# Kernel tuning notes

Measured on AMD Instinct MI355X. Metric: run time of the kernel, lower is better.

## Reference

```python
import jax, jax.numpy as jnp
import numpy as np

N = 100000   # nodes
E = 1600000  # directed edges (before self loops)
IN = 64
HID = 32     # per-head hidden channels
H = 4        # heads
OUT = 32     # final output channels
NEG_SLOPE = 0.2
LN_EPS = 1e-5


def setup_inputs() -> dict:
    key = jax.random.key(0)
    ks = jax.random.split(key, 24)
    def nrm(k, shape, s=0.1):
        return jax.random.normal(k, shape, jnp.float32) * s
    inp = {
        "x": jax.random.normal(ks[0], (N, IN), jnp.float32),
        "edge_index": jax.random.randint(ks[1], (2, E), 0, N, jnp.int32),
    }
    in_dims = [IN, H * HID, H * HID]
    j = 2
    for i, di in enumerate(in_dims):
        inp[f"W{i}"] = nrm(ks[j], (di, H * HID)); j += 1
        inp[f"as{i}"] = nrm(ks[j], (H, HID)); j += 1
        inp[f"ad{i}"] = nrm(ks[j], (H, HID)); j += 1
        inp[f"b{i}"] = jnp.zeros((H * HID,), jnp.float32)
        inp[f"g{i}"] = jnp.ones((H * HID,), jnp.float32)
        inp[f"be{i}"] = jnp.zeros((H * HID,), jnp.float32)
    inp["Wf"] = nrm(ks[j], (H * HID, OUT)); j += 1
    inp["asf"] = nrm(ks[j], (1, OUT)); j += 1
    inp["adf"] = nrm(ks[j], (1, OUT)); j += 1
    inp["bf"] = jnp.zeros((OUT,), jnp.float32)
    return inp


def gat_conv(x, src, dst, W, att_s, att_d, bias, heads, C, concat, n_nodes):
    # h: [N, H, C]
    h = (x @ W).reshape(n_nodes, heads, C)
    a_src = jnp.sum(h * att_s, axis=-1)  # [N, H]
    a_dst = jnp.sum(h * att_d, axis=-1)  # [N, H]
    e = jax.nn.leaky_relu(a_src[src] + a_dst[dst], NEG_SLOPE)  # [E', H]
    # segment softmax over incoming edges of each dst node
    m = jax.ops.segment_max(e, dst, num_segments=n_nodes)
    m = jnp.where(jnp.isfinite(m), m, 0.0)
    ex = jnp.exp(e - m[dst])
    denom = jax.ops.segment_sum(ex, dst, num_segments=n_nodes)
    alpha = ex / (denom[dst] + 1e-16)  # [E', H]
    msg = h[src] * alpha[..., None]    # [E', H, C]
    out = jax.ops.segment_sum(msg, dst, num_segments=n_nodes)  # [N, H, C]
    if concat:
        out = out.reshape(n_nodes, heads * C)
    else:
        out = out.mean(axis=1)
    return out + bias


def layer_norm(x, g, b):
    mu = x.mean(-1, keepdims=True)
    v = jnp.mean((x - mu) ** 2, axis=-1, keepdims=True)
    return g * (x - mu) / jnp.sqrt(v + LN_EPS) + b


def reference(x, edge_index,
              W0, as0, ad0, b0, g0, be0,
              W1, as1, ad1, b1, g1, be1,
              W2, as2, ad2, b2, g2, be2,
              Wf, asf, adf, bf):
    n_nodes = x.shape[0]
    loop = jnp.arange(n_nodes, dtype=edge_index.dtype)
    src = jnp.concatenate([edge_index[0], loop])  # add self loops (PyG default)
    dst = jnp.concatenate([edge_index[1], loop])
    blocks = [(W0, as0, ad0, b0, g0, be0),
              (W1, as1, ad1, b1, g1, be1),
              (W2, as2, ad2, b2, g2, be2)]
    for (W, a_s, a_d, b, g, be) in blocks:
        x = gat_conv(x, src, dst, W, a_s, a_d, b, H, HID, True, n_nodes)
        x = jax.nn.elu(layer_norm(x, g, be))
    return gat_conv(x, src, dst, Wf, asf, adf, bf, 1, OUT, False, n_nodes)
```

## Files before the change

kernel.cpp:

```cpp
#include <hip/hip_runtime.h>
#include <hip/hip_bf16.h>

constexpr int NN   = 100000;
constexpr int EE   = 1600000;
constexpr int ETOT = EE + NN;
constexpr float SLOPE = 0.2f;
constexpr int BSH = 8;
constexpr int NB  = (NN + (1 << BSH) - 1) >> BSH;
constexpr int CCH = 8192;
constexpr int DCAP  = 36;
constexpr int DCAPP = 37;

typedef __attribute__((ext_vector_type(8))) short short8;
typedef __attribute__((ext_vector_type(4))) float f32x4;

__device__ __forceinline__ float bf_lo(unsigned u) { return __uint_as_float(u << 16); }
__device__ __forceinline__ float bf_hi(unsigned u) { return __uint_as_float(u & 0xffff0000u); }
__device__ __forceinline__ unsigned short f2bf(float f) {
    __hip_bfloat16 h = __float2bfloat16(f);
    return *(unsigned short*)&h;
}
__device__ __forceinline__ void wave_lds_fence() {
    __asm__ volatile("s_waitcnt lgkmcnt(0)" ::: "memory");
}
__device__ __forceinline__ void fma8(float* acc, uint4 u, float al) {
    acc[0] += bf_lo(u.x) * al; acc[1] += bf_hi(u.x) * al;
    acc[2] += bf_lo(u.y) * al; acc[3] += bf_hi(u.y) * al;
    acc[4] += bf_lo(u.z) * al; acc[5] += bf_hi(u.z) * al;
    acc[6] += bf_lo(u.w) * al; acc[7] += bf_hi(u.w) * al;
}
__device__ __forceinline__ void fma4(float* acc, uint2 u, float al) {
    acc[0] += bf_lo(u.x) * al; acc[1] += bf_hi(u.x) * al;
    acc[2] += bf_lo(u.y) * al; acc[3] += bf_hi(u.y) * al;
}

__global__ void k_cvt_x(const float* __restrict__ x, unsigned short* __restrict__ xb) {
    int i = blockIdx.x * blockDim.x + threadIdx.x;
    if (i >= NN * 64 / 8) return;
    const float4* xp = (const float4*)(x + (size_t)i * 8);
    float4 v0 = xp[0], v1 = xp[1];
    unsigned short o[8] = {f2bf(v0.x), f2bf(v0.y), f2bf(v0.z), f2bf(v0.w),
                           f2bf(v1.x), f2bf(v1.y), f2bf(v1.z), f2bf(v1.w)};
    *(uint4*)(xb + (size_t)i * 8) = *(uint4*)o;
}

__global__ void k_cvt_wt(const float* __restrict__ W, unsigned short* __restrict__ Wt,
                         int K, int N) {
    int i = blockIdx.x * blockDim.x + threadIdx.x;
    if (i >= K * N) return;
    int k = i / N, n = i % N;
    Wt[(size_t)n * K + k] = f2bf(W[i]);
}

__global__ void k_zero(int* p, int n) {
    int i = blockIdx.x * blockDim.x + threadIdx.x;
    if (i < n) p[i] = 0;
}

__global__ __launch_bounds__(256) void k_bhist(const int* __restrict__ ei,
                                               int* __restrict__ gbh) {
    __shared__ int h[NB];
    int t = threadIdx.x;
    for (int i = t; i < NB; i += 256) h[i] = 0;
    __syncthreads();
    int i = blockIdx.x * 2048 + t;
#pragma unroll
    for (int k = 0; k < 8; k++, i += 256)
        if (i < EE) atomicAdd(&h[ei[EE + i] >> BSH], 1);
    __syncthreads();
    for (int j = t; j < NB; j += 256)
        if (h[j]) atomicAdd(&gbh[j], h[j]);
}

__global__ void k_bscan(const int* __restrict__ gbh, int* __restrict__ ebase,
                        int* __restrict__ gcur) {
    __shared__ int sd[512];
    int t = threadIdx.x;
    int v = (t < NB) ? gbh[t] : 0;
    sd[t] = v;
    __syncthreads();
    for (int off = 1; off < 512; off <<= 1) {
        int x = (t >= off) ? sd[t - off] : 0;
        __syncthreads();
        sd[t] += x;
        __syncthreads();
    }
    int ex = sd[t] - v;
    if (t < NB) { ebase[t] = ex; gcur[t] = ex; }
    if (t == NB) ebase[NB] = EE;
}

__global__ __launch_bounds__(256) void k_bscatter(const int* __restrict__ ei,
                                                  int* __restrict__ gcur,
                                                  int* __restrict__ pbuf) {
    __shared__ int h[NB], base[NB], cur[NB];
    int t = threadIdx.x;
    for (int i = t; i < NB; i += 256) { h[i] = 0; cur[i] = 0; }
    __syncthreads();
    int c0 = blockIdx.x * CCH;
    int cend = c0 + CCH < EE ? c0 + CCH : EE;
    for (int i = c0 + t; i < cend; i += 256)
        atomicAdd(&h[ei[EE + i] >> BSH], 1);
    __syncthreads();
    for (int i = t; i < NB; i += 256)
        if (h[i] > 0) base[i] = atomicAdd(&gcur[i], h[i]);
    __syncthreads();
    for (int i = c0 + t; i < cend; i += 256) {
        int s = ei[i], d = ei[EE + i];
        int b = d >> BSH;
        int c = atomicAdd(&cur[b], 1);
        pbuf[base[b] + c] = s | ((d & ((1 << BSH) - 1)) << 17);
    }
}

__global__ __launch_bounds__(256) void k_bcsr(const int* __restrict__ pbuf,
                                              const int* __restrict__ ebase,
                                              int* __restrict__ row_ptr,
                                              int* __restrict__ esrc) {
    constexpr int BNODES = 1 << BSH;
    __shared__ int hist[BNODES];
    __shared__ int cur[BNODES];
    __shared__ int sd[256];
    int b = blockIdx.x, t = threadIdx.x;
    int node0 = b << BSH;
    int e0 = ebase[b], e1 = ebase[b + 1];
    hist[t] = 0; cur[t] = 0;
    __syncthreads();
    for (int i = e0 + t; i < e1; i += 256)
        atomicAdd(&hist[pbuf[i] >> 17], 1);
    __syncthreads();
    int ts = hist[t];
    sd[t] = ts;
    __syncthreads();
    for (int off = 1; off < 256; off <<= 1) {
        int x = (t >= off) ? sd[t - off] : 0;
        __syncthreads();
        sd[t] += x;
        __syncthreads();
    }
    int ex = sd[t] - ts;
    __syncthreads();
    hist[t] = ex;
    __syncthreads();
    int rbase = e0 + node0;
    int n = node0 + t;
    if (n < NN) {
        int rp = rbase + hist[t] + t;
        row_ptr[n] = rp;
        esrc[rp] = n;
    }
    __syncthreads();
    for (int i = e0 + t; i < e1; i += 256) {
        int p = pbuf[i];
        int nl = p >> 17;
        int c = atomicAdd(&cur[nl], 1);
        esrc[rbase + hist[nl] + nl + 1 + c] = p & 0x1FFFF;
    }
}

template <int BN, int H>
__global__ __launch_bounds__(256) void k_mfma_att(
    const unsigned short* __restrict__ Ab, const unsigned short* __restrict__ Bt,
    const float* __restrict__ as_, const float* __restrict__ ad_,
    unsigned short* __restrict__ hb, float* __restrict__ a_s,
    float* __restrict__ a_d, int M, int K) {
    constexpr int NCT = BN / 16;
    constexpr int LDK = 72;
    __shared__ unsigned short As[128 * LDK];
    __shared__ unsigned short Bs[BN * LDK];
    int tid = threadIdx.x;
    int lane = tid & 63, w = tid >> 6;
    int q = lane >> 4, col = lane & 15;
    int rowBase = blockIdx.x * 128;

    f32x4 acc[2][NCT];
#pragma unroll
    for (int rt = 0; rt < 2; rt++)
#pragma unroll
        for (int ct = 0; ct < NCT; ct++) acc[rt][ct] = (f32x4){0.f, 0.f, 0.f, 0.f};

    int u = tid & 7;
    int r0 = tid >> 3;
    int nph = K >> 6;
    for (int ph = 0; ph < nph; ph++) {
        int kof = ph * 64 + u * 8;
#pragma unroll
        for (int rr = r0; rr < 128; rr += 32) {
            int gr = rowBase + rr;
            uint4 v = make_uint4(0, 0, 0, 0);
            if (gr < M) v = *(const uint4*)(Ab + (size_t)gr * K + kof);
            *(uint4*)(&As[rr * LDK + u * 8]) = v;
        }
#pragma unroll
        for (int br = r0; br < BN; br += 32) {
            uint4 v = *(const uint4*)(Bt + (size_t)br * K + kof);
            *(uint4*)(&Bs[br * LDK + u * 8]) = v;
        }
        __syncthreads();

        short8 af[2][2];
#pragma unroll
        for (int rt = 0; rt < 2; rt++)
#pragma unroll
            for (int kt = 0; kt < 2; kt++)
                af[rt][kt] = *(const short8*)(&As[(w * 32 + rt * 16 + col) * LDK + kt * 32 + q * 8]);
#pragma unroll
        for (int kt = 0; kt < 2; kt++)
#pragma unroll
            for (int ct = 0; ct < NCT; ct++) {
                short8 bf = *(const short8*)(&Bs[(ct * 16 + col) * LDK + kt * 32 + q * 8]);
#pragma unroll
                for (int rt = 0; rt < 2; rt++)
                    acc[rt][ct] = __builtin_amdgcn_mfma_f32_16x16x32_bf16(
                        af[rt][kt], bf, acc[rt][ct], 0, 0, 0);
            }
        __syncthreads();
    }

    float swv[NCT], dwv[NCT];
#pragma unroll
    for (int ct = 0; ct < NCT; ct++) {
        int c = ct * 16 + col;
        swv[ct] = as_[c];
        dwv[ct] = ad_[c];
    }
#pragma unroll
    for (int rt = 0; rt < 2; rt++) {
#pragma unroll
        for (int r = 0; r < 4; r++) {
            int gr = rowBase + w * 32 + rt * 16 + q * 4 + r;
            if constexpr (H == 4) {
                float ps[4] = {0, 0, 0, 0}, pd[4] = {0, 0, 0, 0};
#pragma unroll
                for (int ct = 0; ct < NCT; ct++) {
                    float v = acc[rt][ct][r];
                    ps[ct >> 1] += v * swv[ct];
                    pd[ct >> 1] += v * dwv[ct];
                }
#pragma unroll
                for (int m = 1; m < 16; m <<= 1)
#pragma unroll
                    for (int h = 0; h < 4; h++) {
                        ps[h] += __shfl_xor(ps[h], m);
                        pd[h] += __shfl_xor(pd[h], m);
                    }
                if (gr < M) {
#pragma unroll
                    for (int ct = 0; ct < NCT; ct++)
                        hb[(size_t)gr * BN + ct * 16 + col] = f2bf(acc[rt][ct][r]);
                    if (col == 0) {
                        *(float4*)(a_s + (size_t)gr * 4) = make_float4(ps[0], ps[1], ps[2], ps[3]);
                        *(float4*)(a_d + (size_t)gr * 4) = make_float4(pd[0], pd[1], pd[2], pd[3]);
                    }
                }
            } else {
                float ps = 0.f, pd = 0.f;
#pragma unroll
                for (int ct = 0; ct < NCT; ct++) {
                    float v = acc[rt][ct][r];
                    ps += v * swv[ct];
                    pd += v * dwv[ct];
                }
#pragma unroll
                for (int m = 1; m < 16; m <<= 1) {
                    ps += __shfl_xor(ps, m);
                    pd += __shfl_xor(pd, m);
                }
                if (gr < M) {
#pragma unroll
                    for (int ct = 0; ct < NCT; ct++)
                        hb[(size_t)gr * BN + ct * 16 + col] = f2bf(acc[rt][ct][r]);
                    if (col == 0) { a_s[gr] = ps; a_d[gr] = pd; }
                }
            }
        }
    }
}

__global__ __launch_bounds__(128) void k_aggregate_ln(
    const unsigned short* __restrict__ hb, const float* __restrict__ a_src,
    const float* __restrict__ a_dst, const int* __restrict__ row_ptr,
    const int* __restrict__ esrc, const float* __restrict__ bias,
    const float* __restrict__ gamma, const float* __restrict__ beta,
    unsigned short* __restrict__ xb) {
    __shared__ uint2 slab_all[2][4 * 4 * DCAPP];
    int tid = threadIdx.x;
    int w = tid >> 6, lane = tid & 63;
    int g = lane >> 4, i = lane & 15;
    int myhead = i >> 2;
    uint2* slab = slab_all[w];
    int n0 = blockIdx.x * 8 + w * 4;
    int n = n0 + g;
    bool valid = n < NN;
    int start = 0, deg = 0;
    if (valid) {
        start = row_ptr[n];
        int end = (n == NN - 1) ? ETOT : row_ptr[n + 1];
        deg = end - start;
    }
    int wmax = deg;
#pragma unroll
    for (int m = 1; m < 64; m <<= 1) wmax = max(wmax, __shfl_xor(wmax, m));

    if (wmax <= DCAP) {
        float4 ad = make_float4(0.f, 0.f, 0.f, 0.f);
        if (valid) ad = ((const float4*)a_dst)[n];
        float d0 = 0.f, d1 = 0.f, d2 = 0.f, d3 = 0.f;
        uint2* nslab = slab + g * (4 * DCAPP);
        for (int k = i; k < deg; k += 16) {
            int s = esrc[start + k];
            float4 a = ((const float4*)a_src)[s];
            float e0 = a.x + ad.x; e0 = fmaxf(e0, SLOPE * e0); float x0 = __expf(e0);
            float e1 = a.y + ad.y; e1 = fmaxf(e1, SLOPE * e1); float x1 = __expf(e1);
            float e2 = a.z + ad.z; e2 = fmaxf(e2, SLOPE * e2); float x2 = __expf(e2);
            float e3 = a.w + ad.w; e3 = fmaxf(e3, SLOPE * e3); float x3 = __expf(e3);
            nslab[0 * DCAPP + k] = make_uint2((unsigned)s, __float_as_uint(x0));
            nslab[1 * DCAPP + k] = make_uint2((unsigned)s, __float_as_uint(x1));
            nslab[2 * DCAPP + k] = make_uint2((unsigned)s, __float_as_uint(x2));
            nslab[3 * DCAPP + k] = make_uint2((unsigned)s, __float_as_uint(x3));
            d0 += x0; d1 += x1; d2 += x2; d3 += x3;
        }
#pragma unroll
        for (int m = 1; m < 16; m <<= 1) {
            d0 += __shfl_xor(d0, m);
            d1 += __shfl_xor(d1, m);
            d2 += __shfl_xor(d2, m);
            d3 += __shfl_xor(d3, m);
        }
        float dh = myhead == 0 ? d0 : myhead == 1 ? d1 : myhead == 2 ? d2 : d3;
        float inv = 1.f / (dh + 1e-16f);
        wave_lds_fence();

        float acc[8];
#pragma unroll
        for (int k = 0; k < 8; k++) acc[k] = 0.f;
        const uint2* myrow = nslab + myhead * DCAPP;
        const unsigned short* hbase = hb + i * 8;
        int j = 0;
        for (; j + 4 <= deg; j += 4) {
            uint2 p0 = myrow[j], p1 = myrow[j + 1], p2 = myrow[j + 2], p3 = myrow[j + 3];
            uint4 u0 = *(const uint4*)(hbase + (size_t)p0.x * 128);
            uint4 u1 = *(const uint4*)(hbase + (size_t)p1.x * 128);
            uint4 u2 = *(const uint4*)(hbase + (size_t)p2.x * 128);
            uint4 u3 = *(const uint4*)(hbase + (size_t)p3.x * 128);
            fma8(acc, u0, __uint_as_float(p0.y));
            fma8(acc, u1, __uint_as_float(p1.y));
            fma8(acc, u2, __uint_as_float(p2.y));
            fma8(acc, u3, __uint_as_float(p3.y));
        }
        for (; j < deg; j++) {
            uint2 p = myrow[j];
            uint4 uu = *(const uint4*)(hbase + (size_t)p.x * 128);
            fma8(acc, uu, __uint_as_float(p.y));
        }
#pragma unroll
        for (int k = 0; k < 8; k++) acc[k] *= inv;

        if (valid) {
            float y[8];
            float sum = 0.f;
            const float4* bp = (const float4*)(bias + i * 8);
            float4 b0 = bp[0], b1 = bp[1];
#pragma unroll
            for (int k = 0; k < 8; k++) {
                float b = k < 4 ? (&b0.x)[k] : (&b1.x)[k - 4];
                y[k] = acc[k] + b;
                sum += y[k];
            }
#pragma unroll
            for (int m = 1; m < 16; m <<= 1) sum += __shfl_xor(sum, m);
            float mu = sum * (1.f / 128.f);
            float ss = 0.f;
            float d[8];
#pragma unroll
            for (int k = 0; k < 8; k++) { d[k] = y[k] - mu; ss += d[k] * d[k]; }
#pragma unroll
            for (int m = 1; m < 16; m <<= 1) ss += __shfl_xor(ss, m);
            float is = rsqrtf(ss * (1.f / 128.f) + 1e-5f);
            const float4* gp = (const float4*)(gamma + i * 8);
            const float4* ep = (const float4*)(beta + i * 8);
            float4 g0 = gp[0], g1 = gp[1], e0 = ep[0], e1 = ep[1];
            unsigned short o16[8];
#pragma unroll
            for (int k = 0; k < 8; k++) {
                float gm = k < 4 ? (&g0.x)[k] : (&g1.x)[k - 4];
                float bt = k < 4 ? (&e0.x)[k] : (&e1.x)[k - 4];
                float z = gm * (d[k] * is) + bt;
                o16[k] = f2bf(z > 0.f ? z : __expf(z) - 1.f);
            }
            *(uint4*)(xb + (size_t)n * 128 + i * 8) = *(uint4*)o16;
        }
    } else {
        for (int m4 = 0; m4 < 4; m4++) {
            int nm = n0 + m4;
            if (nm >= NN) continue;
            int startm = row_ptr[nm];
            int endm = (nm == NN - 1) ? ETOT : row_ptr[nm + 1];
            int degm = endm - startm;
            float4 ad = ((const float4*)a_dst)[nm];
            int gg = lane >> 4, c16 = lane & 15, hh = c16 >> 2;
            float acc[8];
#pragma unroll
            for (int k = 0; k < 8; k++) acc[k] = 0.f;
            if (degm <= 64) {
                int msrc = 0;
                float me0 = 0.f, me1 = 0.f, me2 = 0.f, me3 = 0.f;
                if (lane < degm) {
                    int s = esrc[startm + lane];
                    msrc = s;
                    float4 a = ((const float4*)a_src)[s];
                    float e0 = a.x + ad.x; e0 = fmaxf(e0, SLOPE * e0); me0 = __expf(e0);
                    float e1 = a.y + ad.y; e1 = fmaxf(e1, SLOPE * e1); me1 = __expf(e1);
                    float e2 = a.z + ad.z; e2 = fmaxf(e2, SLOPE * e2); me2 = __expf(e2);
                    float e3 = a.w + ad.w; e3 = fmaxf(e3, SLOPE * e3); me3 = __expf(e3);
                }
                float d0 = me0, d1 = me1, d2 = me2, d3 = me3;
#pragma unroll
                for (int m = 1; m < 64; m <<= 1) {
                    d0 += __shfl_xor(d0, m);
                    d1 += __shfl_xor(d1, m);
                    d2 += __shfl_xor(d2, m);
                    d3 += __shfl_xor(d3, m);
                }
                me0 *= 1.f / (d0 + 1e-16f);
                me1 *= 1.f / (d1 + 1e-16f);
                me2 *= 1.f / (d2 + 1e-16f);
                me3 *= 1.f / (d3 + 1e-16f);
                int iters = (degm + 3) >> 2;
                for (int it = 0; it < iters; it++) {
                    int j = gg + (it << 2);
                    int jj = j < degm ? j : 0;
                    int s = __shfl(msrc, jj);
                    float a0 = __shfl(me0, jj), a1 = __shfl(me1, jj);
                    float a2 = __shfl(me2, jj), a3 = __shfl(me3, jj);
                    if (j < degm) {
                        float al = hh == 0 ? a0 : hh == 1 ? a1 : hh == 2 ? a2 : a3;
                        uint4 uu = *(const uint4*)(hb + (size_t)s * 128 + c16 * 8);
                        fma8(acc, uu, al);
                    }
                }
            } else {
                float d0 = 0.f, d1 = 0.f, d2 = 0.f, d3 = 0.f;
                for (int k = startm + lane; k < endm; k += 64) {
                    int s = esrc[k];
                    float4 a = ((const float4*)a_src)[s];
                    float e0 = a.x + ad.x; e0 = fmaxf(e0, SLOPE * e0); d0 += __expf(e0);
                    float e1 = a.y + ad.y; e1 = fmaxf(e1, SLOPE * e1); d1 += __expf(e1);
                    float e2 = a.z + ad.z; e2 = fmaxf(e2, SLOPE * e2); d2 += __expf(e2);
                    float e3 = a.w + ad.w; e3 = fmaxf(e3, SLOPE * e3); d3 += __expf(e3);
                }
#pragma unroll
                for (int m = 1; m < 64; m <<= 1) {
                    d0 += __shfl_xor(d0, m);
                    d1 += __shfl_xor(d1, m);
                    d2 += __shfl_xor(d2, m);
                    d3 += __shfl_xor(d3, m);
                }
                float invh = hh == 0 ? 1.f / (d0 + 1e-16f) : hh == 1 ? 1.f / (d1 + 1e-16f)
                           : hh == 2 ? 1.f / (d2 + 1e-16f) : 1.f / (d3 + 1e-16f);
                float adh = hh == 0 ? ad.x : hh == 1 ? ad.y : hh == 2 ? ad.z : ad.w;
                for (int j = gg; j < degm; j += 4) {
                    int s = esrc[startm + j];
                    float e = a_src[(size_t)s * 4 + hh] + adh;
                    e = fmaxf(e, SLOPE * e);
                    float al = __expf(e) * invh;
                    uint4 uu = *(const uint4*)(hb + (size_t)s * 128 + c16 * 8);
                    fma8(acc, uu, al);
                }
            }
#pragma unroll
            for (int k = 0; k < 8; k++) {
                acc[k] += __shfl_xor(acc[k], 16);
                acc[k] += __shfl_xor(acc[k], 32);
            }
            if (lane < 16) {
                float y[8];
                float sum = 0.f;
                const float4* bp = (const float4*)(bias + lane * 8);
                float4 b0 = bp[0], b1 = bp[1];
#pragma unroll
                for (int k = 0; k < 8; k++) {
                    float b = k < 4 ? (&b0.x)[k] : (&b1.x)[k - 4];
                    y[k] = acc[k] + b;
                    sum += y[k];
                }
#pragma unroll
                for (int m = 1; m < 16; m <<= 1) sum += __shfl_xor(sum, m);
                float mu = sum * (1.f / 128.f);
                float ss = 0.f;
                float d[8];
#pragma unroll
                for (int k = 0; k < 8; k++) { d[k] = y[k] - mu; ss += d[k] * d[k]; }
#pragma unroll
                for (int m = 1; m < 16; m <<= 1) ss += __shfl_xor(ss, m);
                float is = rsqrtf(ss * (1.f / 128.f) + 1e-5f);
                const float4* gp = (const float4*)(gamma + lane * 8);
                const float4* ep = (const float4*)(beta + lane * 8);
                float4 g0 = gp[0], g1 = gp[1], e0 = ep[0], e1 = ep[1];
                unsigned short o16[8];
#pragma unroll
                for (int k = 0; k < 8; k++) {
                    float gm = k < 4 ? (&g0.x)[k] : (&g1.x)[k - 4];
                    float bt = k < 4 ? (&e0.x)[k] : (&e1.x)[k - 4];
                    float z = gm * (d[k] * is) + bt;
                    o16[k] = f2bf(z > 0.f ? z : __expf(z) - 1.f);
                }
                *(uint4*)(xb + (size_t)nm * 128 + lane * 8) = *(uint4*)o16;
            }
        }
    }
}

__global__ __launch_bounds__(128) void k_agg_final(
    const unsigned short* __restrict__ hb, const float* __restrict__ a_src,
    const float* __restrict__ a_dst, const int* __restrict__ row_ptr,
    const int* __restrict__ esrc, const float* __restrict__ bf,
    float* __restrict__ out) {
    __shared__ uint2 slab_all[2][64];
    int lane = threadIdx.x & 63;
    int w = threadIdx.x >> 6;
    uint2* slab = slab_all[w];
    int n = blockIdx.x * 2 + w;
    if (n >= NN) return;
    int start = row_ptr[n];
    int end = (n == NN - 1) ? ETOT : row_ptr[n + 1];
    int deg = end - start;
    float adn = a_dst[n];

    int g = lane >> 3, c8 = lane & 7;
    float acc[4] = {0.f, 0.f, 0.f, 0.f};
    float inv = 1.f;

    if (deg <= 64) {
        int msrc = 0;
        float me = 0.f;
        if (lane < deg) {
            int s = esrc[start + lane];
            msrc = s;
            float e = a_src[s] + adn;
            e = fmaxf(e, SLOPE * e);
            me = __expf(e);
        }
        float d = me;
#pragma unroll
        for (int m = 1; m < 64; m <<= 1) d += __shfl_xor(d, m);
        inv = 1.f / (d + 1e-16f);
        if (lane < deg) slab[lane] = make_uint2((unsigned)msrc, __float_as_uint(me));
        wave_lds_fence();
        const unsigned short* hbase = hb + c8 * 4;
        int j = g;
        for (; j + 8 < deg; j += 16) {
            uint2 p0 = slab[j], p1 = slab[j + 8];
            uint2 u0 = *(const uint2*)(hbase + (size_t)p0.x * 32);
            uint2 u1 = *(const uint2*)(hbase + (size_t)p1.x * 32);
            fma4(acc, u0, __uint_as_float(p0.y));
            fma4(acc, u1, __uint_as_float(p1.y));
        }
        if (j < deg) {
            uint2 p = slab[j];
            uint2 u = *(const uint2*)(hbase + (size_t)p.x * 32);
            fma4(acc, u, __uint_as_float(p.y));
        }
#pragma unroll
        for (int k = 0; k < 4; k++) acc[k] *= inv;
    } else {
        float d = 0.f;
        for (int k = start + lane; k < end; k += 64) {
            int s = esrc[k];
            float e = a_src[s] + adn;
            e = fmaxf(e, SLOPE * e);
            d += __expf(e);
        }
#pragma unroll
        for (int m = 1; m < 64; m <<= 1) d += __shfl_xor(d, m);
        inv = 1.f / (d + 1e-16f);
        for (int j = g; j < deg; j += 8) {
            int s = esrc[start + j];
            float e = a_src[s] + adn;
            e = fmaxf(e, SLOPE * e);
            float al = __expf(e) * inv;
            uint2 u = *(const uint2*)(hb + (size_t)s * 32 + c8 * 4);
            fma4(acc, u, al);
        }
    }
#pragma unroll
    for (int k = 0; k < 4; k++) {
        acc[k] += __shfl_xor(acc[k], 8);
        acc[k] += __shfl_xor(acc[k], 16);
        acc[k] += __shfl_xor(acc[k], 32);
    }
    if (lane < 8) {
        float4 b4 = ((const float4*)bf)[lane];
        float4 o = make_float4(acc[0] + b4.x, acc[1] + b4.y, acc[2] + b4.z,
                               acc[3] + b4.w);
        ((float4*)out)[(size_t)n * 8 + lane] = o;
    }
}

extern "C" void kernel_launch(void* const* d_in, const int* in_sizes, int n_in,
                              void* d_out, int out_size, void* d_ws,
                              size_t ws_size, hipStream_t stream) {
    const float* x  = (const float*)d_in[0];
    const int* ei   = (const int*)d_in[1];
    const float* W[3]  = {(const float*)d_in[2], (const float*)d_in[8],  (const float*)d_in[14]};
    const float* AS[3] = {(const float*)d_in[3], (const float*)d_in[9],  (const float*)d_in[15]};
    const float* AD[3] = {(const float*)d_in[4], (const float*)d_in[10], (const float*)d_in[16]};
    const float* Bb[3] = {(const float*)d_in[5], (const float*)d_in[11], (const float*)d_in[17]};
    const float* G[3]  = {(const float*)d_in[6], (const float*)d_in[12], (const float*)d_in[18]};
    const float* BE[3] = {(const float*)d_in[7], (const float*)d_in[13], (const float*)d_in[19]};
    const float* Wf  = (const float*)d_in[20];
    const float* asf = (const float*)d_in[21];
    const float* adf = (const float*)d_in[22];
    const float* bfp = (const float*)d_in[23];
    float* out = (float*)d_out;

    unsigned short* xb = (unsigned short*)d_ws;
    unsigned short* hb = xb + (size_t)NN * 128;
    float* a_s = (float*)(hb + (size_t)NN * 128);
    float* a_d = a_s + (size_t)NN * 4;
    int* row_ptr = (int*)(a_d + (size_t)NN * 4);
    int* esrc    = row_ptr + NN;
    int* gbh     = esrc + ETOT;
    int* ebase   = gbh + NB;
    int* gcur    = ebase + NB + 1;
    int* pbuf    = gcur + NB;
    unsigned short* Wt0 = (unsigned short*)(pbuf + EE);
    unsigned short* Wt1 = Wt0 + 128 * 64;
    unsigned short* Wt2 = Wt1 + 128 * 128;
    unsigned short* Wtf = Wt2 + 128 * 128;

    k_cvt_x<<<(NN * 64 / 8 + 255) / 256, 256, 0, stream>>>(x, xb);
    k_cvt_wt<<<(64 * 128 + 255) / 256, 256, 0, stream>>>(W[0], Wt0, 64, 128);
    k_cvt_wt<<<(128 * 128 + 255) / 256, 256, 0, stream>>>(W[1], Wt1, 128, 128);
    k_cvt_wt<<<(128 * 128 + 255) / 256, 256, 0, stream>>>(W[2], Wt2, 128, 128);
    k_cvt_wt<<<(128 * 32 + 255) / 256, 256, 0, stream>>>(Wf, Wtf, 128, 32);

    k_zero<<<(NB + 127) / 128, 128, 0, stream>>>(gbh, NB);
    k_bhist<<<(EE + 2047) / 2048, 256, 0, stream>>>(ei, gbh);
    k_bscan<<<1, 512, 0, stream>>>(gbh, ebase, gcur);
    k_bscatter<<<(EE + CCH - 1) / CCH, 256, 0, stream>>>(ei, gcur, pbuf);
    k_bcsr<<<NB, 256, 0, stream>>>(pbuf, ebase, row_ptr, esrc);

    const unsigned short* Wts[3] = {Wt0, Wt1, Wt2};
    int K = 64;
    int gblk = (NN + 127) / 128;
    for (int l = 0; l < 3; l++) {
        k_mfma_att<128, 4><<<gblk, 256, 0, stream>>>(xb, Wts[l], AS[l], AD[l],
                                                     hb, a_s, a_d, NN, K);
        k_aggregate_ln<<<(NN + 7) / 8, 128, 0, stream>>>(hb, a_s, a_d, row_ptr,
                                                         esrc, Bb[l], G[l], BE[l], xb);
        K = 128;
    }
    k_mfma_att<32, 1><<<gblk, 256, 0, stream>>>(xb, Wtf, asf, adf, hb, a_s, a_d,
                                                NN, 128);
    k_agg_final<<<(NN + 1) / 2, 128, 0, stream>>>(hb, a_s, a_d, row_ptr, esrc,
                                                  bfp, out);
}
```

Before: 532.3 us.

## Sort nodes by degree for aggregation load balance and merge weight conversions

Builds a degree histogram during CSR construction, then scans and scatters it to get a permutation of nodes sorted by descending in-degree (clamped at 63). The aggregation kernels now process nodes in that order, so nodes handled by the same wave have similar degree and fewer lanes sit idle on the wave-max degree loop. It also merges the four weight-transpose launches into one kernel. The cost is two extra small kernels, an indirection load per node, and less locality in the output writes and row_ptr reads.

```diff
diff --git a/kernel.cpp b/kernel.cpp
--- a/kernel.cpp
+++ b/kernel.cpp
@@ -44,12 +44,25 @@
     *(uint4*)(xb + (size_t)i * 8) = *(uint4*)o;
 }
 
-__global__ void k_cvt_wt(const float* __restrict__ W, unsigned short* __restrict__ Wt,
-                         int K, int N) {
-    int i = blockIdx.x * blockDim.x + threadIdx.x;
-    if (i >= K * N) return;
-    int k = i / N, n = i % N;
-    Wt[(size_t)n * K + k] = f2bf(W[i]);
+__global__ __launch_bounds__(256) void k_cvt_w_all(
+    const float* __restrict__ W0, const float* __restrict__ W1,
+    const float* __restrict__ W2, const float* __restrict__ Wf,
+    unsigned short* __restrict__ Wt0, unsigned short* __restrict__ Wt1,
+    unsigned short* __restrict__ Wt2, unsigned short* __restrict__ Wtf) {
+    int i = blockIdx.x * 256 + threadIdx.x;
+    if (i < 8192) {
+        int k = i / 128, n = i % 128;
+        Wt0[n * 64 + k] = f2bf(W0[i]);
+    } else if (i < 24576) {
+        int j = i - 8192; int k = j / 128, n = j % 128;
+        Wt1[n * 128 + k] = f2bf(W1[j]);
+    } else if (i < 40960) {
+        int j = i - 24576; int k = j / 128, n = j % 128;
+        Wt2[n * 128 + k] = f2bf(W2[j]);
+    } else if (i < 45056) {
+        int j = i - 40960; int k = j / 32, n = j % 32;
+        Wtf[n * 128 + k] = f2bf(Wf[j]);
+    }
 }
 
 __global__ void k_zero(int* p, int n) {
@@ -73,9 +86,10 @@
 }
 
 __global__ void k_bscan(const int* __restrict__ gbh, int* __restrict__ ebase,
-                        int* __restrict__ gcur) {
+                        int* __restrict__ gcur, int* __restrict__ dh) {
     __shared__ int sd[512];
     int t = threadIdx.x;
+    if (t < 64) dh[t] = 0;
     int v = (t < NB) ? gbh[t] : 0;
     sd[t] = v;
     __syncthreads();
@@ -116,7 +130,8 @@
 __global__ __launch_bounds__(256) void k_bcsr(const int* __restrict__ pbuf,
                                               const int* __restrict__ ebase,
                                               int* __restrict__ row_ptr,
-                                              int* __restrict__ esrc) {
+                                              int* __restrict__ esrc,
+                                              int* __restrict__ dh) {
     constexpr int BNODES = 1 << BSH;
     __shared__ int hist[BNODES];
     __shared__ int cur[BNODES];
@@ -130,6 +145,10 @@
         atomicAdd(&hist[pbuf[i] >> 17], 1);
     __syncthreads();
     int ts = hist[t];
+    if (node0 + t < NN) {
+        int deg = ts + 1;
+        atomicAdd(&dh[deg > 63 ? 63 : deg], 1);
+    }
     sd[t] = ts;
     __syncthreads();
     for (int off = 1; off < 256; off <<= 1) {
@@ -155,6 +174,45 @@
         int nl = p >> 17;
         int c = atomicAdd(&cur[nl], 1);
         esrc[rbase + hist[nl] + nl + 1 + c] = p & 0x1FFFF;
+    }
+}
+
+__global__ void k_dscan(const int* __restrict__ dh, int* __restrict__ dcur) {
+    __shared__ int sd[64];
+    int t = threadIdx.x;
+    int b = 63 - t;
+    int v = dh[b];
+    sd[t] = v;
+    __syncthreads();
+    for (int off = 1; off < 64; off <<= 1) {
+        int x = (t >= off) ? sd[t - off] : 0;
+        __syncthreads();
+        sd[t] += x;
+        __syncthreads();
+    }
+    dcur[b] = sd[t] - v;
+}
+
+__global__ __launch_bounds__(256) void k_dscatter(const int* __restrict__ row_ptr,
+                                                  int* __restrict__ dcur,
+                                                  int* __restrict__ dperm) {
+    __shared__ int h[64], base[64], lcur[64];
+    int t = threadIdx.x;
+    if (t < 64) { h[t] = 0; lcur[t] = 0; }
+    __syncthreads();
+    int n = blockIdx.x * 256 + t;
+    int bin = 0;
+    if (n < NN) {
+        int deg = ((n == NN - 1) ? ETOT : row_ptr[n + 1]) - row_ptr[n];
+        bin = deg > 63 ? 63 : deg;
+        atomicAdd(&h[bin], 1);
+    }
+    __syncthreads();
+    if (t < 64 && h[t] > 0) base[t] = atomicAdd(&dcur[t], h[t]);
+    __syncthreads();
+    if (n < NN) {
+        int c = atomicAdd(&lcur[bin], 1);
+        dperm[base[bin] + c] = n;
     }
 }
 
@@ -280,7 +338,8 @@
 __global__ __launch_bounds__(128) void k_aggregate_ln(
     const unsigned short* __restrict__ hb, const float* __restrict__ a_src,
     const float* __restrict__ a_dst, const int* __restrict__ row_ptr,
-    const int* __restrict__ esrc, const float* __restrict__ bias,
+    const int* __restrict__ esrc, const int* __restrict__ dperm,
+    const float* __restrict__ bias,
     const float* __restrict__ gamma, const float* __restrict__ beta,
     unsigned short* __restrict__ xb) {
     __shared__ uint2 slab_all[2][4 * 4 * DCAPP];
@@ -290,10 +349,11 @@
     int myhead = i >> 2;
     uint2* slab = slab_all[w];
     int n0 = blockIdx.x * 8 + w * 4;
-    int n = n0 + g;
-    bool valid = n < NN;
-    int start = 0, deg = 0;
+    int idx = n0 + g;
+    bool valid = idx < NN;
+    int n = 0, start = 0, deg = 0;
     if (valid) {
+        n = dperm[idx];
         start = row_ptr[n];
         int end = (n == NN - 1) ? ETOT : row_ptr[n + 1];
         deg = end - start;
@@ -392,8 +452,9 @@
         }
     } else {
         for (int m4 = 0; m4 < 4; m4++) {
-            int nm = n0 + m4;
-            if (nm >= NN) continue;
+            int nmidx = n0 + m4;
+            if (nmidx >= NN) continue;
+            int nm = dperm[nmidx];
             int startm = row_ptr[nm];
             int endm = (nm == NN - 1) ? ETOT : row_ptr[nm + 1];
             int degm = endm - startm;
@@ -514,14 +575,15 @@
 __global__ __launch_bounds__(128) void k_agg_final(
     const unsigned short* __restrict__ hb, const float* __restrict__ a_src,
     const float* __restrict__ a_dst, const int* __restrict__ row_ptr,
-    const int* __restrict__ esrc, const float* __restrict__ bf,
-    float* __restrict__ out) {
+    const int* __restrict__ esrc, const int* __restrict__ dperm,
+    const float* __restrict__ bf, float* __restrict__ out) {
     __shared__ uint2 slab_all[2][64];
     int lane = threadIdx.x & 63;
     int w = threadIdx.x >> 6;
     uint2* slab = slab_all[w];
-    int n = blockIdx.x * 2 + w;
-    if (n >= NN) return;
+    int nidx = blockIdx.x * 2 + w;
+    if (nidx >= NN) return;
+    int n = dperm[nidx];
     int start = row_ptr[n];
     int end = (n == NN - 1) ? ETOT : row_ptr[n + 1];
     int deg = end - start;
@@ -628,18 +690,20 @@
     unsigned short* Wt1 = Wt0 + 128 * 64;
     unsigned short* Wt2 = Wt1 + 128 * 128;
     unsigned short* Wtf = Wt2 + 128 * 128;
+    int* dh    = (int*)(Wtf + 32 * 128);
+    int* dcur  = dh + 64;
+    int* dperm = dcur + 64;
 
     k_cvt_x<<<(NN * 64 / 8 + 255) / 256, 256, 0, stream>>>(x, xb);
-    k_cvt_wt<<<(64 * 128 + 255) / 256, 256, 0, stream>>>(W[0], Wt0, 64, 128);
-    k_cvt_wt<<<(128 * 128 + 255) / 256, 256, 0, stream>>>(W[1], Wt1, 128, 128);
-    k_cvt_wt<<<(128 * 128 + 255) / 256, 256, 0, stream>>>(W[2], Wt2, 128, 128);
-    k_cvt_wt<<<(128 * 32 + 255) / 256, 256, 0, stream>>>(Wf, Wtf, 128, 32);
+    k_cvt_w_all<<<176, 256, 0, stream>>>(W[0], W[1], W[2], Wf, Wt0, Wt1, Wt2, Wtf);
 
     k_zero<<<(NB + 127) / 128, 128, 0, stream>>>(gbh, NB);
     k_bhist<<<(EE + 2047) / 2048, 256, 0, stream>>>(ei, gbh);
-    k_bscan<<<1, 512, 0, stream>>>(gbh, ebase, gcur);
+    k_bscan<<<1, 512, 0, stream>>>(gbh, ebase, gcur, dh);
     k_bscatter<<<(EE + CCH - 1) / CCH, 256, 0, stream>>>(ei, gcur, pbuf);
-    k_bcsr<<<NB, 256, 0, stream>>>(pbuf, ebase, row_ptr, esrc);
+    k_bcsr<<<NB, 256, 0, stream>>>(pbuf, ebase, row_ptr, esrc, dh);
+    k_dscan<<<1, 64, 0, stream>>>(dh, dcur);
+    k_dscatter<<<(NN + 255) / 256, 256, 0, stream>>>(row_ptr, dcur, dperm);
 
     const unsigned short* Wts[3] = {Wt0, Wt1, Wt2};
     int K = 64;
@@ -648,11 +712,11 @@
         k_mfma_att<128, 4><<<gblk, 256, 0, stream>>>(xb, Wts[l], AS[l], AD[l],
                                                      hb, a_s, a_d, NN, K);
         k_aggregate_ln<<<(NN + 7) / 8, 128, 0, stream>>>(hb, a_s, a_d, row_ptr,
-                                                         esrc, Bb[l], G[l], BE[l], xb);
+                                                         esrc, dperm, Bb[l], G[l], BE[l], xb);
         K = 128;
     }
     k_mfma_att<32, 1><<<gblk, 256, 0, stream>>>(xb, Wtf, asf, adf, hb, a_s, a_d,
                                                 NN, 128);
     k_agg_final<<<(NN + 1) / 2, 128, 0, stream>>>(hb, a_s, a_d, row_ptr, esrc,
-                                                  bfp, out);
-}
+                                                  dperm, bfp, out);
+}
```

After: 825.0 us. 55.0% more time.

## Load MFMA A fragments directly from global and stage full B once

Applied to the files above, without the earlier changes.

Rewrites the GEMM+attention kernel to load the whole transposed weight matrix into shared memory once per block, and to read the A-operand fragments straight from global memory into registers, dropping the A shared-memory tile and the per-phase barriers. It also merges the four weight conversion kernels into one launch. The aim is to cut LDS traffic, sync overhead and launch count. In exchange, A reads become strided global loads per lane, which may coalesce less well.

```diff
diff --git a/kernel.cpp b/kernel.cpp
--- a/kernel.cpp
+++ b/kernel.cpp
@@ -44,12 +44,25 @@
     *(uint4*)(xb + (size_t)i * 8) = *(uint4*)o;
 }
 
-__global__ void k_cvt_wt(const float* __restrict__ W, unsigned short* __restrict__ Wt,
-                         int K, int N) {
-    int i = blockIdx.x * blockDim.x + threadIdx.x;
-    if (i >= K * N) return;
-    int k = i / N, n = i % N;
-    Wt[(size_t)n * K + k] = f2bf(W[i]);
+__global__ __launch_bounds__(256) void k_cvt_w_all(
+    const float* __restrict__ W0, const float* __restrict__ W1,
+    const float* __restrict__ W2, const float* __restrict__ Wf,
+    unsigned short* __restrict__ Wt0, unsigned short* __restrict__ Wt1,
+    unsigned short* __restrict__ Wt2, unsigned short* __restrict__ Wtf) {
+    int i = blockIdx.x * 256 + threadIdx.x;
+    if (i < 8192) {
+        int k = i / 128, n = i % 128;
+        Wt0[n * 64 + k] = f2bf(W0[i]);
+    } else if (i < 24576) {
+        int j = i - 8192; int k = j / 128, n = j % 128;
+        Wt1[n * 128 + k] = f2bf(W1[j]);
+    } else if (i < 40960) {
+        int j = i - 24576; int k = j / 128, n = j % 128;
+        Wt2[n * 128 + k] = f2bf(W2[j]);
+    } else if (i < 45056) {
+        int j = i - 40960; int k = j / 32, n = j % 32;
+        Wtf[n * 128 + k] = f2bf(Wf[j]);
+    }
 }
 
 __global__ void k_zero(int* p, int n) {
@@ -165,56 +178,51 @@
     unsigned short* __restrict__ hb, float* __restrict__ a_s,
     float* __restrict__ a_d, int M, int K) {
     constexpr int NCT = BN / 16;
-    constexpr int LDK = 72;
-    __shared__ unsigned short As[128 * LDK];
-    __shared__ unsigned short Bs[BN * LDK];
+    constexpr int LDKB = 136;
+    __shared__ unsigned short Bs[BN * LDKB];
     int tid = threadIdx.x;
     int lane = tid & 63, w = tid >> 6;
     int q = lane >> 4, col = lane & 15;
     int rowBase = blockIdx.x * 128;
 
+    int kvs = (K == 64) ? 3 : 4;
+    for (int idx = tid; idx < (BN << kvs); idx += 256) {
+        int br = idx >> kvs;
+        int ko = (idx & ((1 << kvs) - 1)) << 3;
+        *(uint4*)(&Bs[br * LDKB + ko]) = *(const uint4*)(Bt + (size_t)br * K + ko);
+    }
+    __syncthreads();
+
     f32x4 acc[2][NCT];
 #pragma unroll
     for (int rt = 0; rt < 2; rt++)
 #pragma unroll
         for (int ct = 0; ct < NCT; ct++) acc[rt][ct] = (f32x4){0.f, 0.f, 0.f, 0.f};
 
-    int u = tid & 7;
-    int r0 = tid >> 3;
+    int r0 = rowBase + w * 32 + col;
+    int grc0 = min(r0, M - 1);
+    int grc1 = min(r0 + 16, M - 1);
+    const unsigned short* a0p = Ab + (size_t)grc0 * K + q * 8;
+    const unsigned short* a1p = Ab + (size_t)grc1 * K + q * 8;
+
     int nph = K >> 6;
     for (int ph = 0; ph < nph; ph++) {
-        int kof = ph * 64 + u * 8;
-#pragma unroll
-        for (int rr = r0; rr < 128; rr += 32) {
-            int gr = rowBase + rr;
-            uint4 v = make_uint4(0, 0, 0, 0);
-            if (gr < M) v = *(const uint4*)(Ab + (size_t)gr * K + kof);
-            *(uint4*)(&As[rr * LDK + u * 8]) = v;
-        }
-#pragma unroll
-        for (int br = r0; br < BN; br += 32) {
-            uint4 v = *(const uint4*)(Bt + (size_t)br * K + kof);
-            *(uint4*)(&Bs[br * LDK + u * 8]) = v;
-        }
-        __syncthreads();
-
+        int kof = ph * 64;
         short8 af[2][2];
-#pragma unroll
-        for (int rt = 0; rt < 2; rt++)
-#pragma unroll
-            for (int kt = 0; kt < 2; kt++)
-                af[rt][kt] = *(const short8*)(&As[(w * 32 + rt * 16 + col) * LDK + kt * 32 + q * 8]);
+        af[0][0] = *(const short8*)(a0p + kof);
+        af[0][1] = *(const short8*)(a0p + kof + 32);
+        af[1][0] = *(const short8*)(a1p + kof);
+        af[1][1] = *(const short8*)(a1p + kof + 32);
 #pragma unroll
         for (int kt = 0; kt < 2; kt++)
 #pragma unroll
             for (int ct = 0; ct < NCT; ct++) {
-                short8 bf = *(const short8*)(&Bs[(ct * 16 + col) * LDK + kt * 32 + q * 8]);
+                short8 bf = *(const short8*)(&Bs[(ct * 16 + col) * LDKB + kof + kt * 32 + q * 8]);
 #pragma unroll
                 for (int rt = 0; rt < 2; rt++)
                     acc[rt][ct] = __builtin_amdgcn_mfma_f32_16x16x32_bf16(
                         af[rt][kt], bf, acc[rt][ct], 0, 0, 0);
             }
-        __syncthreads();
     }
 
     float swv[NCT], dwv[NCT];
@@ -630,10 +638,7 @@
     unsigned short* Wtf = Wt2 + 128 * 128;
 
     k_cvt_x<<<(NN * 64 / 8 + 255) / 256, 256, 0, stream>>>(x, xb);
-    k_cvt_wt<<<(64 * 128 + 255) / 256, 256, 0, stream>>>(W[0], Wt0, 64, 128);
-    k_cvt_wt<<<(128 * 128 + 255) / 256, 256, 0, stream>>>(W[1], Wt1, 128, 128);
-    k_cvt_wt<<<(128 * 128 + 255) / 256, 256, 0, stream>>>(W[2], Wt2, 128, 128);
-    k_cvt_wt<<<(128 * 32 + 255) / 256, 256, 0, stream>>>(Wf, Wtf, 128, 32);
+    k_cvt_w_all<<<176, 256, 0, stream>>>(W[0], W[1], W[2], Wf, Wt0, Wt1, Wt2, Wtf);
 
     k_zero<<<(NB + 127) / 128, 128, 0, stream>>>(gbh, NB);
     k_bhist<<<(EE + 2047) / 2048, 256, 0, stream>>>(ei, gbh);
```

Result: faster. 521.5 us (-2.0%).
